# Optimization experiments

Measured on AMD Instinct MI355X. Metric: run time of the kernel, lower is better.

The kernel has to match this reference:

```python
import jax, jax.numpy as jnp
import numpy as np

NUM_HEADS = 16
DIM_IN = 1024
DIM_Q = 64
DIM_K = 64


def setup_inputs() -> dict:
    key = jax.random.key(0)
    ks = jax.random.split(key, 12)
    B, S = 4, 2048
    s_in = 1.0 / np.sqrt(DIM_IN)
    s_o = 1.0 / np.sqrt(NUM_HEADS * DIM_K)
    return {
        "Q": jax.random.normal(ks[0], (B, S, DIM_IN), jnp.float32),
        "K": jax.random.normal(ks[1], (B, S, DIM_IN), jnp.float32),
        "V": jax.random.normal(ks[2], (B, S, DIM_IN), jnp.float32),
        # per-head projection weights stacked along head axis
        "Wq": jax.random.uniform(ks[3], (NUM_HEADS, DIM_IN, DIM_Q), jnp.float32, -s_in, s_in),
        "bq": jax.random.uniform(ks[4], (NUM_HEADS, DIM_Q), jnp.float32, -s_in, s_in),
        "Wk": jax.random.uniform(ks[5], (NUM_HEADS, DIM_IN, DIM_K), jnp.float32, -s_in, s_in),
        "bk": jax.random.uniform(ks[6], (NUM_HEADS, DIM_K), jnp.float32, -s_in, s_in),
        "Wv": jax.random.uniform(ks[7], (NUM_HEADS, DIM_IN, DIM_K), jnp.float32, -s_in, s_in),
        "bv": jax.random.uniform(ks[8], (NUM_HEADS, DIM_K), jnp.float32, -s_in, s_in),
        # output projection: (num_heads*dim_k) -> dim_in
        "Wo": jax.random.uniform(ks[9], (NUM_HEADS * DIM_K, DIM_IN), jnp.float32, -s_o, s_o),
        "bo": jax.random.uniform(ks[10], (DIM_IN,), jnp.float32, -s_o, s_o),
    }


def reference(Q, K, V, Wq, bq, Wk, bk, Wv, bv, Wo, bo):
    # Batched across heads: equivalent to the per-head Python loop in the
    # original module (heads concatenated along the feature dim in order).
    q = jnp.einsum("bsd,hdq->bhsq", Q, Wq) + bq[None, :, None, :]  # [B,H,S,dq]
    k = jnp.einsum("btd,hdq->bhtq", K, Wk) + bk[None, :, None, :]  # [B,H,T,dk]
    v = jnp.einsum("btd,hdv->bhtv", V, Wv) + bv[None, :, None, :]  # [B,H,T,dv]
    scale = 1.0 / jnp.sqrt(jnp.asarray(q.shape[-1], q.dtype))
    scores = jnp.einsum("bhsq,bhtq->bhst", q, k) * scale           # [B,H,S,T]
    attn = jax.nn.softmax(scores, axis=-1)
    out = jnp.einsum("bhst,bhtv->bhsv", attn, v)                   # [B,H,S,dv]
    B, H, S, Dv = out.shape
    concat = jnp.transpose(out, (0, 2, 1, 3)).reshape(B, S, H * Dv)  # torch.cat(dim=2)
    return concat @ Wo + bo
```

## Files before the change

### kernel.cpp

```cpp
#include <hip/hip_runtime.h>

typedef short bf16x8 __attribute__((ext_vector_type(8)));
typedef float f32x4 __attribute__((ext_vector_type(4)));

#define MFMA16(a, b, c) __builtin_amdgcn_mfma_f32_16x16x32_bf16(a, b, c, 0, 0, 0)

#define SC 0.18033688011112043f

__device__ __forceinline__ unsigned short f2bf(float f) {
  union { float f; unsigned u; } v; v.f = f;
  unsigned r = v.u + 0x7FFFu + ((v.u >> 16) & 1u);
  return (unsigned short)(r >> 16);
}

__device__ __forceinline__ float exp2_fast(float x) {
  float r;
  asm("v_exp_f32 %0, %1" : "=v"(r) : "v"(x));
  return r;
}

typedef __attribute__((address_space(1))) const unsigned int gas_u32;
typedef __attribute__((address_space(3))) unsigned int las_u32;
__device__ __forceinline__ void glds16(const void* g, void* l) {
  __builtin_amdgcn_global_load_lds((gas_u32*)g, (las_u32*)l, 16, 0, 0);
}

template<int NSRC>
__global__ void tcvt_kernel(const float* __restrict__ s0p, const float* __restrict__ s1p,
                            const float* __restrict__ s2p, unsigned short* __restrict__ d0p,
                            unsigned short* __restrict__ d1p, unsigned short* __restrict__ d2p,
                            int R, int C) {
  __shared__ float tile[64][65];
  int z = blockIdx.z, mat = 0, zz = z;
  if (NSRC == 3) { mat = z >> 4; zz = z & 15; }
  const float* s = (mat == 0 ? s0p : (mat == 1 ? s1p : s2p)) + (size_t)zz * R * C;
  unsigned short* d = (mat == 0 ? d0p : (mat == 1 ? d1p : d2p)) + (size_t)zz * R * C;
  int r0 = blockIdx.x << 6, c0 = blockIdx.y << 6;
  int t = threadIdx.x;
  int lr = t >> 2, lc = (t & 3) << 4;
#pragma unroll
  for (int j = 0; j < 16; j += 4) {
    float4 v = *(const float4*)(s + (size_t)(r0 + lr) * C + c0 + lc + j);
    tile[lr][lc + j + 0] = v.x; tile[lr][lc + j + 1] = v.y;
    tile[lr][lc + j + 2] = v.z; tile[lr][lc + j + 3] = v.w;
  }
  __syncthreads();
  int oc = t >> 2, orr = (t & 3) << 4;
  unsigned short* dp = d + (size_t)(c0 + oc) * R + r0 + orr;
#pragma unroll
  for (int jj = 0; jj < 4; ++jj) {
    ushort4 o;
    o.x = f2bf(tile[orr + (jj << 2) + 0][oc]);
    o.y = f2bf(tile[orr + (jj << 2) + 1][oc]);
    o.z = f2bf(tile[orr + (jj << 2) + 2][oc]);
    o.w = f2bf(tile[orr + (jj << 2) + 3][oc]);
    *(ushort4*)(dp + (jj << 2)) = o;
  }
}

__global__ __launch_bounds__(256, 2)
void gemm_qkv_kernel(const float* __restrict__ Qf, const float* __restrict__ Kf,
                     const float* __restrict__ Vf,
                     const unsigned short* __restrict__ Wt,
                     const float* __restrict__ bq, const float* __restrict__ bk,
                     const float* __restrict__ bv,
                     unsigned short* __restrict__ qbuf,
                     unsigned short* __restrict__ kbuf,
                     unsigned short* __restrict__ vtbuf) {
  __shared__ __align__(16) char ldsc[49152];
  float* lds_a32 = (float*)ldsc;
  unsigned short* lds_b = (unsigned short*)(ldsc + 32768);
  const int tid = threadIdx.x;
  const int w = tid >> 6, l = tid & 63;
  const int g = l >> 4, x = l & 15;
  const int wm = (w >> 1) << 6, wn = (w & 1) << 6;
  const int bid = blockIdx.x;
  const int xcd = bid & 7, slot = bid >> 3;
  const int sec = slot >> 6;
  const int inner = slot & 63;
  const int m0 = ((xcd << 3) + (inner >> 3)) << 7;
  const int n0 = (inner & 7) << 7;
  const int nt = (sec << 3) + (inner & 7);
  const float* A = sec == 0 ? Qf : (sec == 1 ? Kf : Vf);
  const unsigned short* W = Wt + ((size_t)nt << 17);
  const float* bias = sec == 0 ? bq : (sec == 1 ? bk : bv);
  const int lrow = l >> 3;
  const int lchk = (l & 7) ^ (lrow & 7);
  const int rl4 = l >> 4;
  const int c16 = l & 15;
  const int offEf = (c16 ^ rl4) << 2;
  const float* baseA0 = A + ((size_t)(m0 + rl4) << 10) + offEf;
  const float* baseA1 = A + ((size_t)(m0 + rl4) << 10) + (offEf ^ 16);
  f32x4 acc[4][4] = {};
  for (int k0 = 0; k0 < 1024; k0 += 64) {
    __syncthreads();
#pragma unroll
    for (int p = 0; p < 8; ++p) {
      int rb = (w << 5) + (p << 2);
      const float* src = ((p & 1) ? baseA1 : baseA0) + ((size_t)rb << 10) + k0;
      glds16(src, (char*)lds_a32 + rb * 256);
    }
#pragma unroll
    for (int p = 0; p < 4; ++p) {
      int rb = (w << 5) + (p << 3);
      glds16(W + ((size_t)(rb + lrow) << 10) + k0 + (lchk << 3),
             (char*)lds_b + rb * 128);
    }
    __syncthreads();
#pragma unroll
    for (int kk = 0; kk < 2; ++kk) {
      bf16x8 af[4], bfr[4];
#pragma unroll
      for (int i = 0; i < 4; ++i) {
        int m = wm + (i << 4) + x;
        const char* ar = (const char*)lds_a32 + m * 256;
        int ba = ((kk << 7) | (g << 5)) ^ ((m & 7) << 4);
        f32x4 lo = *(const f32x4*)(ar + ba);
        f32x4 hi = *(const f32x4*)(ar + (ba ^ 16));
        union { unsigned u[4]; bf16x8 v; } cu;
        asm("v_cvt_pk_bf16_f32 %0, %1, %2" : "=v"(cu.u[0]) : "v"(lo[0]), "v"(lo[1]));
        asm("v_cvt_pk_bf16_f32 %0, %1, %2" : "=v"(cu.u[1]) : "v"(lo[2]), "v"(lo[3]));
        asm("v_cvt_pk_bf16_f32 %0, %1, %2" : "=v"(cu.u[2]) : "v"(hi[0]), "v"(hi[1]));
        asm("v_cvt_pk_bf16_f32 %0, %1, %2" : "=v"(cu.u[3]) : "v"(hi[2]), "v"(hi[3]));
        af[i] = cu.v;
        int n = wn + (i << 4) + x;
        bfr[i] = *(const bf16x8*)((const char*)lds_b + n * 128 +
                                  (((kk << 6) + (g << 4)) ^ ((n & 7) << 4)));
      }
#pragma unroll
      for (int i = 0; i < 4; ++i)
#pragma unroll
        for (int j = 0; j < 4; ++j)
          acc[i][j] = MFMA16(af[i], bfr[j], acc[i][j]);
    }
  }

  if (sec < 2) {
    unsigned short* dst = sec == 0 ? qbuf : kbuf;
    const float scale = sec == 0 ? SC : 1.0f;
#pragma unroll
    for (int j = 0; j < 4; ++j) {
      int n = n0 + wn + (j << 4) + x;
      float bv2 = bias[n];
      int h = n >> 6, dd = n & 63;
#pragma unroll
      for (int i = 0; i < 4; ++i) {
#pragma unroll
        for (int r = 0; r < 4; ++r) {
          int M = m0 + wm + (i << 4) + (g << 2) + r;
          int b = M >> 11, s = M & 2047;
          dst[(size_t)(b * 16 + h) * 131072 + (size_t)s * 64 + dd] =
              f2bf((acc[i][j][r] + bv2) * scale);
        }
      }
    }
  } else {
    __syncthreads();
#pragma unroll
    for (int i = 0; i < 4; ++i)
#pragma unroll
      for (int j = 0; j < 4; ++j) {
        int nl = wn + (j << 4) + x;
        float bv2 = bias[n0 + nl];
        ushort4 pk;
        pk.x = f2bf(acc[i][j][0] + bv2);
        pk.y = f2bf(acc[i][j][1] + bv2);
        pk.z = f2bf(acc[i][j][2] + bv2);
        pk.w = f2bf(acc[i][j][3] + bv2);
        int ml = wm + (i << 4) + (g << 2);
        *(ushort4*)(ldsc + nl * 256 + ((ml * 2) ^ ((nl & 7) << 4))) = pk;
      }
    __syncthreads();
    int nl = tid >> 1, half = tid & 1;
    int n = n0 + nl, h = n >> 6, dd = n & 63;
    int bb = m0 >> 11;
    size_t base = ((size_t)(bb * 16 + h) * 64 + dd) * 2048 + (m0 & 2047) + (half << 6);
#pragma unroll
    for (int c = 0; c < 8; ++c) {
      int mb = (half << 7) + (c << 4);
      uint4 vv = *(const uint4*)(ldsc + nl * 256 + (mb ^ ((nl & 7) << 4)));
      *(uint4*)(vtbuf + base + (c << 3)) = vv;
    }
  }
}

__global__ __launch_bounds__(256, 2)
void gemm_o_kernel(const unsigned short* __restrict__ A,
                   const unsigned short* __restrict__ W,
                   const float* __restrict__ bias,
                   float* __restrict__ dst) {
  __shared__ unsigned short lds[16384];
  unsigned short* lds_a = lds;
  unsigned short* lds_b = lds + 8192;
  const int tid = threadIdx.x;
  const int w = tid >> 6, l = tid & 63;
  const int g = l >> 4, x = l & 15;
  const int wm = (w >> 1) << 6, wn = (w & 1) << 6;
  const int bid = blockIdx.x;
  const int xcd = bid & 7, slot = bid >> 3;
  const int m0 = ((xcd << 3) + (slot & 7)) << 7;
  const int n0 = (slot >> 3) << 7;
  const int lrow = l >> 3;
  const int lchk = (l & 7) ^ (lrow & 7);
  f32x4 acc[4][4] = {};
  for (int k0 = 0; k0 < 1024; k0 += 64) {
    __syncthreads();
#pragma unroll
    for (int p = 0; p < 4; ++p) {
      int rb = (w << 5) + (p << 3);
      glds16(A + ((size_t)(m0 + rb + lrow) << 10) + k0 + (lchk << 3),
             (char*)lds_a + rb * 128);
      glds16(W + ((size_t)(n0 + rb + lrow) << 10) + k0 + (lchk << 3),
             (char*)lds_b + rb * 128);
    }
    __syncthreads();
#pragma unroll
    for (int kk = 0; kk < 2; ++kk) {
      bf16x8 af[4], bfr[4];
#pragma unroll
      for (int i = 0; i < 4; ++i) {
        int m = wm + (i << 4) + x;
        af[i] = *(const bf16x8*)((const char*)lds_a + m * 128 +
                                 (((kk << 6) + (g << 4)) ^ ((m & 7) << 4)));
        int n = wn + (i << 4) + x;
        bfr[i] = *(const bf16x8*)((const char*)lds_b + n * 128 +
                                  (((kk << 6) + (g << 4)) ^ ((n & 7) << 4)));
      }
#pragma unroll
      for (int i = 0; i < 4; ++i)
#pragma unroll
        for (int j = 0; j < 4; ++j)
          acc[i][j] = MFMA16(af[i], bfr[j], acc[i][j]);
    }
  }
#pragma unroll
  for (int j = 0; j < 4; ++j) {
    int n = n0 + wn + (j << 4) + x;
    float bv = bias[n];
#pragma unroll
    for (int i = 0; i < 4; ++i) {
#pragma unroll
      for (int r = 0; r < 4; ++r) {
        int M = m0 + wm + (i << 4) + (g << 2) + r;
        dst[(size_t)M * 1024 + n] = acc[i][j][r] + bv;
      }
    }
  }
}

__device__ __forceinline__ void softmax_pack(const f32x4* s, bf16x8& o0, bf16x8& o1) {
  unsigned pk[4][2];
#pragma unroll
  for (int tt = 0; tt < 4; ++tt) {
    float p0 = exp2_fast(s[tt][0]);
    float p1 = exp2_fast(s[tt][1]);
    float p2 = exp2_fast(s[tt][2]);
    float p3 = exp2_fast(s[tt][3]);
    asm("v_cvt_pk_bf16_f32 %0, %1, %2" : "=v"(pk[tt][0]) : "v"(p0), "v"(p1));
    asm("v_cvt_pk_bf16_f32 %0, %1, %2" : "=v"(pk[tt][1]) : "v"(p2), "v"(p3));
  }
  union { unsigned u[4]; bf16x8 v; } w0, w1;
#pragma unroll
  for (int p = 0; p < 2; ++p) {
    unsigned X = pk[0][p], Y = pk[1][p];
    asm("v_permlane32_swap_b32 %0, %1" : "+v"(X), "+v"(Y));
    asm("v_permlane16_swap_b32 %0, %1" : "+v"(X), "+v"(Y));
    w0.u[p] = X; w0.u[2 + p] = Y;
    unsigned X2 = pk[2][p], Y2 = pk[3][p];
    asm("v_permlane32_swap_b32 %0, %1" : "+v"(X2), "+v"(Y2));
    asm("v_permlane16_swap_b32 %0, %1" : "+v"(X2), "+v"(Y2));
    w1.u[p] = X2; w1.u[2 + p] = Y2;
  }
  o0 = w0.v; o1 = w1.v;
}

__global__ __attribute__((amdgpu_flat_work_group_size(512, 512), amdgpu_waves_per_eu(4, 8)))
void flash_kernel(const unsigned short* __restrict__ qb,
                  const unsigned short* __restrict__ kb,
                  const unsigned short* __restrict__ vtb,
                  unsigned short* __restrict__ out) {
  __shared__ unsigned short lds_k[2][4096];
  __shared__ unsigned short lds_v[2][4096];
  const int tid = threadIdx.x, w = tid >> 6, l = tid & 63;
  const int g = l >> 4, x = l & 15;
  const int bid = blockIdx.x;
  const int xcd = bid & 7, slot = bid >> 3;
  const int bh = (xcd << 3) + (slot >> 3);
  const int s0 = (slot & 7) << 8;
  const size_t boff = (size_t)bh << 17;
  const int str = tid >> 3, stc = (tid & 7) << 3;
  const int swb = str * 128 + ((stc << 1) ^ ((str & 7) << 4));
  const unsigned short* ksrc = kb + boff + ((size_t)str << 6) + stc;
  const unsigned short* vsrc = vtb + boff + ((size_t)str << 11) + stc;
  const bf16x8 ones = {(short)0x3F80, (short)0x3F80, (short)0x3F80, (short)0x3F80,
                       (short)0x3F80, (short)0x3F80, (short)0x3F80, (short)0x3F80};
  bf16x8 qf0[2], qf1[2];
#pragma unroll
  for (int i = 0; i < 2; ++i) {
    const unsigned short* qp = qb + boff + ((size_t)(s0 + (w << 5) + (i << 4) + x) << 6);
    qf0[i] = *(const bf16x8*)(qp + (g << 3));
    qf1[i] = *(const bf16x8*)(qp + 32 + (g << 3));
  }
  f32x4 accA[4] = {}, accB[4] = {};
  f32x4 accSA = {}, accSB = {};
  {
    uint4 kv = *(const uint4*)ksrc;
    uint4 vv = *(const uint4*)vsrc;
    *(uint4*)((char*)lds_k[0] + swb) = kv;
    *(uint4*)((char*)lds_v[0] + swb) = vv;
  }
  __syncthreads();
  int cur = 0;
  for (int t0 = 0; t0 < 2048; t0 += 64) {
    const bool more = t0 < 1984;
    uint4 nk, nv;
    if (more) {
      nk = *(const uint4*)(ksrc + ((size_t)(t0 + 64) << 6));
      nv = *(const uint4*)(vsrc + t0 + 64);
    }
    f32x4 sA[4], sB[4];
#pragma unroll
    for (int tt = 0; tt < 4; ++tt) {
      int trow = (tt << 4) + x;
      const char* kr = (const char*)lds_k[cur] + trow * 128;
      int sw = (trow & 7) << 4;
      bf16x8 k0 = *(const bf16x8*)(kr + ((g << 4) ^ sw));
      bf16x8 k1 = *(const bf16x8*)(kr + ((64 + (g << 4)) ^ sw));
      __builtin_amdgcn_s_setprio(1);
      f32x4 t4 = {};
      t4 = MFMA16(k0, qf0[0], t4);
      t4 = MFMA16(k1, qf1[0], t4);
      sA[tt] = t4;
      f32x4 u4 = {};
      u4 = MFMA16(k0, qf0[1], u4);
      u4 = MFMA16(k1, qf1[1], u4);
      sB[tt] = u4;
      __builtin_amdgcn_s_setprio(0);
    }
    bf16x8 paA[2], paB[2];
    softmax_pack(sA, paA[0], paA[1]);
    softmax_pack(sB, paB[0], paB[1]);
    __builtin_amdgcn_s_setprio(1);
    accSA = MFMA16(paA[0], ones, accSA);
    accSA = MFMA16(paA[1], ones, accSA);
    accSB = MFMA16(paB[0], ones, accSB);
    accSB = MFMA16(paB[1], ones, accSB);
    __builtin_amdgcn_s_setprio(0);
#pragma unroll
    for (int kk = 0; kk < 2; ++kk) {
#pragma unroll
      for (int nn = 0; nn < 4; ++nn) {
        int dv = (nn << 4) + x;
        bf16x8 vb = *(const bf16x8*)((const char*)lds_v[cur] + dv * 128 +
                                     (((kk << 6) + (g << 4)) ^ ((dv & 7) << 4)));
        __builtin_amdgcn_s_setprio(1);
        accA[nn] = MFMA16(paA[kk], vb, accA[nn]);
        accB[nn] = MFMA16(paB[kk], vb, accB[nn]);
        __builtin_amdgcn_s_setprio(0);
      }
    }
    if (more) {
      int nb = cur ^ 1;
      *(uint4*)((char*)lds_k[nb] + swb) = nk;
      *(uint4*)((char*)lds_v[nb] + swb) = nv;
    }
    __syncthreads();
    cur ^= 1;
  }
  const int b = bh >> 4, h = bh & 15;
#pragma unroll
  for (int i = 0; i < 2; ++i) {
    f32x4& as = i == 0 ? accSA : accSB;
    f32x4* ac = i == 0 ? accA : accB;
    float iv[4];
#pragma unroll
    for (int r = 0; r < 4; ++r) iv[r] = 1.f / as[r];
    const int srow = s0 + (w << 5) + (i << 4) + (g << 2);
#pragma unroll
    for (int nn = 0; nn < 4; ++nn) {
      int dv = (nn << 4) + x;
      size_t base = ((size_t)(b * 2048 + srow)) * 1024 + (h << 6) + dv;
      out[base]        = f2bf(ac[nn][0] * iv[0]);
      out[base + 1024] = f2bf(ac[nn][1] * iv[1]);
      out[base + 2048] = f2bf(ac[nn][2] * iv[2]);
      out[base + 3072] = f2bf(ac[nn][3] * iv[3]);
    }
  }
}

extern "C" void kernel_launch(void* const* d_in, const int* in_sizes, int n_in,
                              void* d_out, int out_size, void* d_ws, size_t ws_size,
                              hipStream_t stream) {
  const float* Q  = (const float*)d_in[0];
  const float* K  = (const float*)d_in[1];
  const float* V  = (const float*)d_in[2];
  const float* Wq = (const float*)d_in[3];
  const float* bq = (const float*)d_in[4];
  const float* Wk = (const float*)d_in[5];
  const float* bk = (const float*)d_in[6];
  const float* Wv = (const float*)d_in[7];
  const float* bv = (const float*)d_in[8];
  const float* Wo = (const float*)d_in[9];
  const float* bo = (const float*)d_in[10];

  if (ws_size < 109051904u) return;

  char* ws = (char*)d_ws;
  unsigned short* concat = (unsigned short*)(ws + 0);
  unsigned short* Wtq   = (unsigned short*)(ws + 50331648);
  unsigned short* Wtk   = (unsigned short*)(ws + 52428800);
  unsigned short* Wtv   = (unsigned short*)(ws + 54525952);
  unsigned short* Wot   = (unsigned short*)(ws + 56623104);
  unsigned short* qbuf  = (unsigned short*)(ws + 58720256);
  unsigned short* kbuf  = (unsigned short*)(ws + 75497472);
  unsigned short* vtbuf = (unsigned short*)(ws + 92274688);

  tcvt_kernel<3><<<dim3(16, 1, 48), 256, 0, stream>>>(Wq, Wk, Wv, Wtq, Wtk, Wtv, 1024, 64);
  tcvt_kernel<1><<<dim3(16, 16, 1), 256, 0, stream>>>(Wo, Wo, Wo, Wot, Wot, Wot, 1024, 1024);
  gemm_qkv_kernel<<<1536, 256, 0, stream>>>(Q, K, V, Wtq, bq, bk, bv, qbuf, kbuf, vtbuf);
  flash_kernel<<<512, 512, 0, stream>>>(qbuf, kbuf, vtbuf, concat);
  gemm_o_kernel<<<512, 256, 0, stream>>>(concat, Wot, bo, (float*)d_out);
}
```

Baseline: 184.2 us.

## Convert QKV activations to bf16 before LDS staging and raise occupancy

The QKV projection GEMM used to copy fp32 activation tiles straight into LDS with global_load_lds, then convert them to bf16 on every fragment read. It now loads fp32 into registers, converts once to bf16, and stores a swizzled bf16 tile. This halves the A-tile LDS footprint (48KB to 32KB total), which allows the launch bound to rise to 3 blocks per CU. The cost is that the asynchronous direct-to-LDS path for A becomes synchronous register loads, which may expose more global memory latency.

```diff
diff --git a/kernel.cpp b/kernel.cpp
--- a/kernel.cpp
+++ b/kernel.cpp
@@ -58,7 +58,7 @@
   }
 }
 
-__global__ __launch_bounds__(256, 2)
+__global__ __launch_bounds__(256, 3)
 void gemm_qkv_kernel(const float* __restrict__ Qf, const float* __restrict__ Kf,
                      const float* __restrict__ Vf,
                      const unsigned short* __restrict__ Wt,
@@ -67,9 +67,9 @@
                      unsigned short* __restrict__ qbuf,
                      unsigned short* __restrict__ kbuf,
                      unsigned short* __restrict__ vtbuf) {
-  __shared__ __align__(16) char ldsc[49152];
-  float* lds_a32 = (float*)ldsc;
-  unsigned short* lds_b = (unsigned short*)(ldsc + 32768);
+  __shared__ __align__(16) char ldsc[32768];
+  unsigned short* lds_a = (unsigned short*)ldsc;
+  unsigned short* lds_b = (unsigned short*)(ldsc + 16384);
   const int tid = threadIdx.x;
   const int w = tid >> 6, l = tid & 63;
   const int g = l >> 4, x = l & 15;
@@ -85,27 +85,31 @@
   const unsigned short* W = Wt + ((size_t)nt << 17);
   const float* bias = sec == 0 ? bq : (sec == 1 ? bk : bv);
   const int lrow = l >> 3;
-  const int lchk = (l & 7) ^ (lrow & 7);
-  const int rl4 = l >> 4;
-  const int c16 = l & 15;
-  const int offEf = (c16 ^ rl4) << 2;
-  const float* baseA0 = A + ((size_t)(m0 + rl4) << 10) + offEf;
-  const float* baseA1 = A + ((size_t)(m0 + rl4) << 10) + (offEf ^ 16);
+  const int lchk = (l & 7) ^ lrow;
+  const int ac = l & 7;
+  const float* aSrc = A + ((size_t)(m0 + (w << 5) + lrow) << 10) + (ac << 3);
+  char* aDst = ldsc + (((w << 5) + lrow) << 7) + ((ac ^ lrow) << 4);
   f32x4 acc[4][4] = {};
   for (int k0 = 0; k0 < 1024; k0 += 64) {
     __syncthreads();
-#pragma unroll
-    for (int p = 0; p < 8; ++p) {
-      int rb = (w << 5) + (p << 2);
-      const float* src = ((p & 1) ? baseA1 : baseA0) + ((size_t)rb << 10) + k0;
-      glds16(src, (char*)lds_a32 + rb * 256);
-    }
 #pragma unroll
     for (int p = 0; p < 4; ++p) {
       int rb = (w << 5) + (p << 3);
       glds16(W + ((size_t)(rb + lrow) << 10) + k0 + (lchk << 3),
              (char*)lds_b + rb * 128);
     }
+#pragma unroll
+    for (int p = 0; p < 4; ++p) {
+      const float* s = aSrc + ((size_t)p << 13) + k0;
+      float4 f0 = *(const float4*)s;
+      float4 f1 = *(const float4*)(s + 4);
+      union { unsigned u[4]; uint4 q; } cu;
+      asm("v_cvt_pk_bf16_f32 %0, %1, %2" : "=v"(cu.u[0]) : "v"(f0.x), "v"(f0.y));
+      asm("v_cvt_pk_bf16_f32 %0, %1, %2" : "=v"(cu.u[1]) : "v"(f0.z), "v"(f0.w));
+      asm("v_cvt_pk_bf16_f32 %0, %1, %2" : "=v"(cu.u[2]) : "v"(f1.x), "v"(f1.y));
+      asm("v_cvt_pk_bf16_f32 %0, %1, %2" : "=v"(cu.u[3]) : "v"(f1.z), "v"(f1.w));
+      *(uint4*)(aDst + (p << 10)) = cu.q;
+    }
     __syncthreads();
 #pragma unroll
     for (int kk = 0; kk < 2; ++kk) {
@@ -113,16 +117,8 @@
 #pragma unroll
       for (int i = 0; i < 4; ++i) {
         int m = wm + (i << 4) + x;
-        const char* ar = (const char*)lds_a32 + m * 256;
-        int ba = ((kk << 7) | (g << 5)) ^ ((m & 7) << 4);
-        f32x4 lo = *(const f32x4*)(ar + ba);
-        f32x4 hi = *(const f32x4*)(ar + (ba ^ 16));
-        union { unsigned u[4]; bf16x8 v; } cu;
-        asm("v_cvt_pk_bf16_f32 %0, %1, %2" : "=v"(cu.u[0]) : "v"(lo[0]), "v"(lo[1]));
-        asm("v_cvt_pk_bf16_f32 %0, %1, %2" : "=v"(cu.u[1]) : "v"(lo[2]), "v"(lo[3]));
-        asm("v_cvt_pk_bf16_f32 %0, %1, %2" : "=v"(cu.u[2]) : "v"(hi[0]), "v"(hi[1]));
-        asm("v_cvt_pk_bf16_f32 %0, %1, %2" : "=v"(cu.u[3]) : "v"(hi[2]), "v"(hi[3]));
-        af[i] = cu.v;
+        af[i] = *(const bf16x8*)((const char*)lds_a + m * 128 +
+                                 (((kk << 6) + (g << 4)) ^ ((m & 7) << 4)));
         int n = wn + (i << 4) + x;
         bfr[i] = *(const bf16x8*)((const char*)lds_b + n * 128 +
                                   (((kk << 6) + (g << 4)) ^ ((n & 7) << 4)));
```

Result: slower. 216.9 us (+17.7%).
